# Kernel optimization log

Measured on AMD Instinct MI355X. Metric: run time of the kernel, lower is better.

The kernel has to match this reference:

```python
import jax, jax.numpy as jnp
import numpy as np
from jax import lax

QMAX = 127.0
EPS = 1e-8

T, B, I, H, L = 1024, 16, 1024, 1024, 2


def setup_inputs() -> dict:
    key = jax.random.key(0)
    ks = jax.random.split(key, 16)
    d = {
        "x": jax.random.normal(ks[0], (T, B, I), jnp.float32),
        "h0": jnp.zeros((L, B, H), jnp.float32),
        "c0": jnp.zeros((L, B, H), jnp.float32),
    }
    # layer 0 weights
    d["w_ih0"] = jax.random.normal(ks[1], (4 * H, I), jnp.float32) * 0.05
    d["w_hh0"] = jax.random.normal(ks[2], (4 * H, H), jnp.float32) * 0.05
    d["b_ih0"] = jax.random.normal(ks[3], (4 * H,), jnp.float32) * 0.05
    d["b_hh0"] = jax.random.normal(ks[4], (4 * H,), jnp.float32) * 0.05
    # layer 1 weights (layer_input_size == hidden_size)
    d["w_ih1"] = jax.random.normal(ks[5], (4 * H, H), jnp.float32) * 0.05
    d["w_hh1"] = jax.random.normal(ks[6], (4 * H, H), jnp.float32) * 0.05
    d["b_ih1"] = jax.random.normal(ks[7], (4 * H,), jnp.float32) * 0.05
    d["b_hh1"] = jax.random.normal(ks[8], (4 * H,), jnp.float32) * 0.05
    return d


def _quantize_weight(w):
    # per-tensor symmetric int8 quantization (simulates quantized.linear_prepack)
    s = jnp.maximum(jnp.max(jnp.abs(w)), EPS) / QMAX
    wq = jnp.clip(jnp.round(w / s), -QMAX, QMAX)  # integer values held in fp32
    return wq, s


def _dynq_matmul(x, wq, w_scale):
    # dynamic per-tensor activation quantization + int8xint8 matmul (fp32-emulated)
    x_scale = jnp.maximum(jnp.max(jnp.abs(x)), EPS) / QMAX
    xq = jnp.clip(jnp.round(x / x_scale), -QMAX, QMAX)
    return (xq @ wq.T) * (x_scale * w_scale)


def _lstm_layer(x, h0, c0, w_ih, w_hh, b_ih, b_hh):
    wq_ih, s_ih = _quantize_weight(w_ih)
    wq_hh, s_hh = _quantize_weight(w_hh)

    def step(carry, xt):
        h, c = carry
        gates = (_dynq_matmul(xt, wq_ih, s_ih) + b_ih
                 + _dynq_matmul(h, wq_hh, s_hh) + b_hh)  # [B, 4H]
        i, f, g, o = jnp.split(gates, 4, axis=-1)  # PyTorch gate order i,f,g,o
        i, f, o = jax.nn.sigmoid(i), jax.nn.sigmoid(f), jax.nn.sigmoid(o)
        g = jnp.tanh(g)
        c_new = f * c + i * g
        h_new = o * jnp.tanh(c_new)
        return (h_new, c_new), h_new

    (hT, cT), ys = lax.scan(step, (h0, c0), x)
    return ys, hT, cT


def reference(x, h0, c0, w_ih0, w_hh0, b_ih0, b_hh0, w_ih1, w_hh1, b_ih1, b_hh1):
    y, h_l0, c_l0 = _lstm_layer(x, h0[0], c0[0], w_ih0, w_hh0, b_ih0, b_hh0)
    y, h_l1, c_l1 = _lstm_layer(y, h0[1], c0[1], w_ih1, w_hh1, b_ih1, b_hh1)
    h_n = jnp.stack([h_l0, h_l1], axis=0)  # [L, B, H]
    c_n = jnp.stack([c_l0, c_l1], axis=0)
    return y, h_n, c_n
```

## Files before the change

kernel.cpp:

```cpp
#include <hip/hip_runtime.h>


#define T_STEPS 1024

typedef int v4i __attribute__((ext_vector_type(4)));
typedef float v4f __attribute__((ext_vector_type(4)));
typedef unsigned v2u __attribute__((ext_vector_type(2)));

#define DEV static __device__ __forceinline__

DEV float qclip(float v) { return fminf(fmaxf(v, -127.0f), 127.0f); }

DEV unsigned pack4i(float a, float b, float c, float d) {
  int ia = (int)a, ib = (int)b, ic = (int)c, id = (int)d;
  return (unsigned)(ia & 0xff) | ((unsigned)(ib & 0xff) << 8) |
         ((unsigned)(ic & 0xff) << 16) | ((unsigned)(id & 0xff) << 24);
}

DEV float qdiv(float v, float s) { return qclip(rintf(v / s)); }
DEV float qmul(float v, float inv) { return qclip(rintf(v * inv)); }

DEV v4i cloadi(const void* p) {
  v4i r;
  asm volatile("global_load_dwordx4 %0, %1, off sc0 sc1" : "=v"(r) : "v"(p) : "memory");
  return r;
}
DEV v4f cloadf(const void* p) {
  v4f r;
  asm volatile("global_load_dwordx4 %0, %1, off sc0 sc1" : "=v"(r) : "v"(p) : "memory");
  return r;
}
DEV unsigned cload4(const void* p) {
  unsigned r;
  asm volatile("global_load_dword %0, %1, off sc0 sc1" : "=v"(r) : "v"(p) : "memory");
  return r;
}
DEV v2u cload8w(const void* p) {
  v2u r;
  asm volatile("global_load_dwordx2 %0, %1, off sc0 sc1\n\ts_waitcnt vmcnt(0)"
               : "=v"(r) : "v"(p) : "memory");
  return r;
}
DEV void cstore16(void* p, v4f v) {
  asm volatile("global_store_dwordx4 %0, %1, off sc0 sc1" :: "v"(p), "v"(v) : "memory");
}
DEV void cstore8(void* p, v2u v) {
  asm volatile("global_store_dwordx2 %0, %1, off sc0 sc1" :: "v"(p), "v"(v) : "memory");
}
DEV void cstore4u(void* p, unsigned v) {
  asm volatile("global_store_dword %0, %1, off sc0 sc1" :: "v"(p), "v"(v) : "memory");
}
DEV void cstore4f(void* p, float v) {
  asm volatile("global_store_dword %0, %1, off sc0 sc1" :: "v"(p), "v"(v) : "memory");
}
DEV void vdone() {
  asm volatile("s_waitcnt vmcnt(0)" ::: "memory");
  __builtin_amdgcn_sched_barrier(0);
}

#define MFMA_I8 __builtin_amdgcn_mfma_i32_16x16x64_i8

__global__ void init_kernel(const float* __restrict__ h0in, char* __restrict__ ws) {
  const int layer = blockIdx.x;
  const int tid = threadIdx.x;
  const float* src = h0in + layer * 16384;
  char* ring = ws + (layer ? 196608 : 65536) + 65536;
  v2u* pubs = (v2u*)(ws + (layer ? 640 : 128)) + 32;
  for (int d = tid; d < 4096; d += 256) {
    int lb = d >> 7, b = (d >> 3) & 15, cq = (d & 7) << 2;
    v4f v = *(const v4f*)(src + (b << 10) + (lb << 5) + cq);
    cstore16(ring + ((size_t)d << 4), v);
  }
  __shared__ float red[256];
  const int lb = tid >> 3, su = tid & 7;
  float m = 0.0f;
  for (int b = su * 2; b < su * 2 + 2; ++b)
    for (int q = 0; q < 32; ++q) m = fmaxf(m, fabsf(src[b * 1024 + lb * 32 + q]));
  red[tid] = m;
  __syncthreads();
  if (su == 0) {
    float mm = red[tid];
#pragma unroll
    for (int i = 1; i < 8; ++i) mm = fmaxf(mm, red[tid + i]);
    v2u p;
    p.x = 0u;
    p.y = __float_as_uint(mm);
    cstore8((char*)&pubs[lb], p);
  }
}

__global__ void wabsmax_kernel(const float* __restrict__ w0, const float* __restrict__ w1,
                               const float* __restrict__ w2, const float* __restrict__ w3,
                               unsigned* wmax) {
  const int tensor = blockIdx.x >> 8;
  const int blk = blockIdx.x & 255;
  const float* w = tensor == 0 ? w0 : tensor == 1 ? w1 : tensor == 2 ? w2 : w3;
  const int tid = threadIdx.x;
  const float4* src = (const float4*)w;
  float m = 0.0f;
#pragma unroll
  for (int i = 0; i < 16; ++i) {
    float4 v = src[blk * 4096 + (i << 8) + tid];
    m = fmaxf(m, fmaxf(fmaxf(fabsf(v.x), fabsf(v.y)), fmaxf(fabsf(v.z), fabsf(v.w))));
  }
  __shared__ float red[256];
  red[tid] = m;
  __syncthreads();
  for (int off = 128; off > 0; off >>= 1) {
    if (tid < off) red[tid] = fmaxf(red[tid], red[tid + off]);
    __syncthreads();
  }
  if (tid == 0)
    __hip_atomic_fetch_max(&wmax[tensor], __float_as_uint(red[0]),
                           __ATOMIC_RELAXED, __HIP_MEMORY_SCOPE_AGENT);
}

__global__ void wquant_kernel(const float* __restrict__ w0, const float* __restrict__ w1,
                              const float* __restrict__ w2, const float* __restrict__ w3,
                              const unsigned* __restrict__ wmax,
                              unsigned char* __restrict__ wq) {
  const int tensor = blockIdx.x >> 12;
  const int blk = blockIdx.x & 4095;
  const float* w = tensor == 0 ? w0 : tensor == 1 ? w1 : tensor == 2 ? w2 : w3;
  const float s = fmaxf(__uint_as_float(wmax[tensor]), 1e-8f) / 127.0f;
  const int f4 = (blk << 8) + threadIdx.x;
  float4 v = ((const float4*)w)[f4];
  unsigned* dst = (unsigned*)(wq + (size_t)tensor * 4194304u);
  dst[f4] = pack4i(qdiv(v.x, s), qdiv(v.y, s), qdiv(v.z, s), qdiv(v.w, s));
}

__global__ void xquant_kernel(const float* __restrict__ x, float* __restrict__ xscale,
                              unsigned char* __restrict__ xq) {
  const int t = blockIdx.x;
  const int tid = threadIdx.x;
  const float4* src = (const float4*)(x + (size_t)t * 16384u);
  float4 vb[16];
  float m = 0.0f;
#pragma unroll
  for (int i = 0; i < 16; ++i) {
    float4 v = src[(i << 8) + tid];
    vb[i] = v;
    m = fmaxf(m, fmaxf(fmaxf(fabsf(v.x), fabsf(v.y)), fmaxf(fabsf(v.z), fabsf(v.w))));
  }
  __shared__ float red[256];
  red[tid] = m;
  __syncthreads();
  for (int off = 128; off > 0; off >>= 1) {
    if (tid < off) red[tid] = fmaxf(red[tid], red[tid + off]);
    __syncthreads();
  }
  __shared__ float ssh;
  if (tid == 0) {
    float s = fmaxf(red[0], 1e-8f) / 127.0f;
    xscale[t] = s;
    ssh = s;
  }
  __syncthreads();
  const float s = ssh;
  unsigned char* dst = xq + ((size_t)t << 14);
  const int kk = tid >> 4;
  const int hi = (tid >> 2) & 3;
  const int jo = (tid & 3) << 2;
#pragma unroll
  for (int i = 0; i < 16; ++i) {
    float4 v = vb[i];
    unsigned q = pack4i(qdiv(v.x, s), qdiv(v.y, s), qdiv(v.z, s), qdiv(v.w, s));
    *(unsigned*)(dst + (kk << 10) + ((i | (hi << 4)) << 4) + jo) = q;
  }
}

__global__ __launch_bounds__(512, 2) void seq_kernel(
    const unsigned char* __restrict__ xq, const float* __restrict__ xscale,
    const unsigned char* __restrict__ wq_base, const unsigned* __restrict__ wmax,
    const float* __restrict__ bih0, const float* __restrict__ bhh0,
    const float* __restrict__ bih1, const float* __restrict__ bhh1,
    char* __restrict__ ws, const float* __restrict__ c0in, float* __restrict__ dout) {
  const int blk = blockIdx.x;
  const int layer = blk >> 5;
  const int lb = blk & 31;
  const int j0 = lb << 5;
  const int tid = threadIdx.x;
  const int w = tid >> 6;
  const int lane = tid & 63;
  const int gate = (lane >> 2) & 3;
  const int unit_l = (w << 2) + (lane & 3);
  const int b0 = (lane >> 4) << 2;

  v2u* pubs0 = (v2u*)(ws + 128);
  v2u* pubs1 = (v2u*)(ws + 640);
  float* hmax0f = (float*)(ws + 4096);
  char* h0f = ws + 65536;
  char* h1f = ws + 196608;
  char* h0qp = ws + 327680;

  __shared__ __align__(16) unsigned char ahq[16][1040];
  __shared__ __align__(16) unsigned char axq[16][1040];
  __shared__ float hstash[16][33];
  __shared__ float redw[8];

  const unsigned char* wqi = wq_base + (size_t)(2 * layer) * 4194304u;
  const unsigned char* wqh = wq_base + (size_t)(2 * layer + 1) * 4194304u;
  const float s_wi = fmaxf(__uint_as_float(wmax[2 * layer + 0]), 1e-8f) / 127.0f;
  const float s_wh = fmaxf(__uint_as_float(wmax[2 * layer + 1]), 1e-8f) / 127.0f;

  const int ncol = (gate << 10) + j0 + unit_l;
  const int ksub = (lane >> 4) << 4;
  const int arow = lane & 15;
  const int gbase = lane & ~12;

  v4i wfi[16], wfh[16];
  {
    const unsigned char* pi = wqi + (size_t)ncol * 1024u + ksub;
    const unsigned char* ph = wqh + (size_t)ncol * 1024u + ksub;
#pragma unroll
    for (int kk = 0; kk < 16; ++kk) {
      wfi[kk] = *(const v4i*)(pi + (kk << 6));
      wfh[kk] = *(const v4i*)(ph + (kk << 6));
    }
  }
  const float bsum = (layer ? bih1 : bih0)[ncol] + (layer ? bhh1 : bhh0)[ncol];

  float cr[4];
#pragma unroll
  for (int r = 0; r < 4; ++r) cr[r] = c0in[(layer << 14) + ((b0 + r) << 10) + j0 + unit_l];

  float bm = 0.f;

  if (layer == 0) {
    for (int s = 0; s <= T_STEPS; ++s) {
      const bool full = (s < T_STEPS);
      v4i ax0 = {0, 0, 0, 0}, ax1 = {0, 0, 0, 0};
      float sxs = 0.f;
      if (full) {
        sxs = xscale[s];
        const unsigned char* xb = xq + ((size_t)s << 14) + (lane << 4);
        v4i xa[8];
#pragma unroll
        for (int kk = 0; kk < 8; ++kk) xa[kk] = *(const v4i*)(xb + (kk << 10));
#pragma unroll
        for (int kk = 0; kk < 8; kk += 2) {
          ax0 = MFMA_I8(xa[kk], wfi[kk], ax0, 0, 0, 0);
          ax1 = MFMA_I8(xa[kk + 1], wfi[kk + 1], ax1, 0, 0, 0);
        }
#pragma unroll
        for (int kk = 0; kk < 8; ++kk) xa[kk] = *(const v4i*)(xb + ((kk + 8) << 10));
#pragma unroll
        for (int kk = 0; kk < 8; kk += 2) {
          ax0 = MFMA_I8(xa[kk], wfi[kk + 8], ax0, 0, 0, 0);
          ax1 = MFMA_I8(xa[kk + 1], wfi[kk + 9], ax1, 0, 0, 0);
        }
      }
      const int slot = (s + 1) & 1;
      const v2u* pp = (lane < 32) ? (pubs0 + (slot << 5) + lane)
                                  : (pubs1 + (slot << 5) + (lane - 32));
      const unsigned tgt = (lane < 32) ? (unsigned)s
                                       : ((s >= 9) ? (unsigned)(s - 8) : 0u);
      v2u pv;
      unsigned guard = 0;
      for (;;) {
        pv = cload8w(pp);
        if (__ballot(pv.x >= tgt) == ~0ull) break;
        __builtin_amdgcn_s_sleep(1);
        if (++guard > (1u << 20)) break;
      }
      const char* hsrc = h0f + (size_t)slot * 65536;
      v4f hv[8];
#pragma unroll
      for (int i = 0; i < 8; ++i) hv[i] = cloadf(hsrc + (i << 13) + (tid << 4));
      float pm = __uint_as_float(pv.y);
#pragma unroll
      for (int m = 1; m < 32; m <<= 1) pm = fmaxf(pm, __shfl_xor(pm, m));
      const float gmax = __shfl(pm, 0);
      const float sh = fmaxf(gmax, 1e-8f) / 127.0f;
      const float inv = 1.0f / sh;
      vdone();
#pragma unroll
      for (int i = 0; i < 8; ++i) {
        unsigned uq = pack4i(qmul(hv[i].x, inv), qmul(hv[i].y, inv),
                             qmul(hv[i].z, inv), qmul(hv[i].w, inv));
        int o = (i << 13) + (tid << 4);
        int lbs = o >> 11, b = (o >> 7) & 15, c = (o & 127) >> 2;
        *(unsigned*)&ahq[b][(lbs << 5) + c] = uq;
      }
      __syncthreads();
      if (s > 0) {
        if (tid < 128) {
          int b = tid >> 3, c = (tid & 7) << 2;
          unsigned uq = *(const unsigned*)&ahq[b][j0 + c];
          cstore4u(h0qp + (size_t)((s - 1) & 7) * 16384 + (lb << 9) + (b << 5) + c, uq);
        }
        if (lb == 0 && tid == 256) cstore4f(&hmax0f[s - 1], gmax);
      }
      if (full) {
        v4i ah0 = {0, 0, 0, 0}, ah1 = {0, 0, 0, 0};
#pragma unroll
        for (int kk = 0; kk < 16; kk += 2) {
          v4i a = *(const v4i*)&ahq[arow][(kk << 6) + ksub];
          v4i b = *(const v4i*)&ahq[arow][((kk + 1) << 6) + ksub];
          ah0 = MFMA_I8(a, wfh[kk], ah0, 0, 0, 0);
          ah1 = MFMA_I8(b, wfh[kk + 1], ah1, 0, 0, 0);
        }
        const float fx = sxs * s_wi, fh = sh * s_wh;
        float am = 0.f;
#pragma unroll
        for (int r = 0; r < 4; ++r) {
          float gv = (float)(ax0[r] + ax1[r]) * fx + (float)(ah0[r] + ah1[r]) * fh + bsum;
          float xxv = (gate == 2) ? 2.f * gv : gv;
          float sg = __fdividef(1.f, 1.f + __expf(-xxv));
          float act = (gate == 2) ? 2.f * sg - 1.f : sg;
          float gi = __shfl(act, gbase);
          float gf = __shfl(act, gbase | 4);
          float gg = __shfl(act, gbase | 8);
          float go = __shfl(act, gbase | 12);
          float cn = gf * cr[r] + gi * gg;
          cr[r] = cn;
          float h = go * (2.f * __fdividef(1.f, 1.f + __expf(-2.f * cn)) - 1.f);
          if (gate == 0) hstash[b0 + r][unit_l] = h;
          am = fmaxf(am, fabsf(h));
        }
#pragma unroll
        for (int m = 1; m < 64; m <<= 1) am = fmaxf(am, __shfl_xor(am, m));
        if (lane == 0) redw[w] = am;
        __syncthreads();
        if (tid < 128) {
          int b = tid >> 3, c = (tid & 7) << 2;
          v4f hw = {hstash[b][c], hstash[b][c + 1], hstash[b][c + 2], hstash[b][c + 3]};
          cstore16(h0f + (size_t)(s & 1) * 65536 + (lb << 11) + (b << 7) + (c << 2), hw);
          if (s == T_STEPS - 1)
            *(v4f*)(dout + 16777216u + (b << 10) + j0 + c) = hw;
        }
        if (tid == 0) {
          bm = redw[0];
#pragma unroll
          for (int i = 1; i < 8; ++i) bm = fmaxf(bm, redw[i]);
        }
      }
      vdone();
      __syncthreads();
      if (tid == 0) {
        v2u pub;
        pub.x = (unsigned)(s + 1);
        pub.y = __float_as_uint(bm);
        cstore8((char*)(pubs0 + ((s & 1) << 5) + lb), pub);
      }
    }
    if (gate == 0) {
#pragma unroll
      for (int r = 0; r < 4; ++r)
        dout[16777216u + 32768u + ((b0 + r) << 10) + j0 + unit_l] = cr[r];
    }
  } else {
    for (int u = 0; u < T_STEPS; ++u) {
      const int slot = (u + 1) & 1;
      const v2u* pp = (lane < 32) ? (pubs0 + (slot << 5) + lane)
                                  : (pubs1 + (slot << 5) + (lane - 32));
      const unsigned tgt = (lane < 32) ? (unsigned)(u + 2) : (unsigned)u;
      v2u pv;
      unsigned guard = 0;
      for (;;) {
        pv = cload8w(pp);
        if (__ballot(pv.x >= tgt) == ~0ull) break;
        __builtin_amdgcn_s_sleep(1);
        if (++guard > (1u << 20)) break;
      }
      const char* qsrc = h0qp + (size_t)(u & 7) * 16384;
      v4i q0 = cloadi(qsrc + (tid << 4));
      v4i q1 = cloadi(qsrc + 8192 + (tid << 4));
      const char* hsrc = h1f + (size_t)slot * 65536;
      v4f hv[8];
#pragma unroll
      for (int i = 0; i < 8; ++i) hv[i] = cloadf(hsrc + (i << 13) + (tid << 4));
      unsigned sxb = cload4(&hmax0f[u]);
      float pm = __uint_as_float(pv.y);
#pragma unroll
      for (int m = 1; m < 32; m <<= 1) pm = fmaxf(pm, __shfl_xor(pm, m));
      const float gmax1 = __shfl(pm, 32);
      const float sh = fmaxf(gmax1, 1e-8f) / 127.0f;
      const float inv = 1.0f / sh;
      vdone();
      const float sxs = fmaxf(__uint_as_float(sxb), 1e-8f) / 127.0f;
      {
        int o = tid << 4;
        *(v4i*)&axq[(o >> 5) & 15][((o >> 9) << 5) + (o & 31)] = q0;
        int o1 = o + 8192;
        *(v4i*)&axq[(o1 >> 5) & 15][((o1 >> 9) << 5) + (o1 & 31)] = q1;
      }
#pragma unroll
      for (int i = 0; i < 8; ++i) {
        unsigned uq = pack4i(qmul(hv[i].x, inv), qmul(hv[i].y, inv),
                             qmul(hv[i].z, inv), qmul(hv[i].w, inv));
        int o = (i << 13) + (tid << 4);
        int lbs = o >> 11, b = (o >> 7) & 15, c = (o & 127) >> 2;
        *(unsigned*)&ahq[b][(lbs << 5) + c] = uq;
      }
      __syncthreads();
      v4i ax0 = {0, 0, 0, 0}, ax1 = {0, 0, 0, 0};
      v4i ah0 = {0, 0, 0, 0}, ah1 = {0, 0, 0, 0};
#pragma unroll
      for (int kk = 0; kk < 16; kk += 2) {
        v4i a0 = *(const v4i*)&axq[arow][(kk << 6) + ksub];
        v4i a1 = *(const v4i*)&axq[arow][((kk + 1) << 6) + ksub];
        v4i b0v = *(const v4i*)&ahq[arow][(kk << 6) + ksub];
        v4i b1v = *(const v4i*)&ahq[arow][((kk + 1) << 6) + ksub];
        ax0 = MFMA_I8(a0, wfi[kk], ax0, 0, 0, 0);
        ax1 = MFMA_I8(a1, wfi[kk + 1], ax1, 0, 0, 0);
        ah0 = MFMA_I8(b0v, wfh[kk], ah0, 0, 0, 0);
        ah1 = MFMA_I8(b1v, wfh[kk + 1], ah1, 0, 0, 0);
      }
      const float fx = sxs * s_wi, fh = sh * s_wh;
      float am = 0.f;
#pragma unroll
      for (int r = 0; r < 4; ++r) {
        float gv = (float)(ax0[r] + ax1[r]) * fx + (float)(ah0[r] + ah1[r]) * fh + bsum;
        float xxv = (gate == 2) ? 2.f * gv : gv;
        float sg = __fdividef(1.f, 1.f + __expf(-xxv));
        float act = (gate == 2) ? 2.f * sg - 1.f : sg;
        float gi = __shfl(act, gbase);
        float gf = __shfl(act, gbase | 4);
        float gg = __shfl(act, gbase | 8);
        float go = __shfl(act, gbase | 12);
        float cn = gf * cr[r] + gi * gg;
        cr[r] = cn;
        float h = go * (2.f * __fdividef(1.f, 1.f + __expf(-2.f * cn)) - 1.f);
        if (gate == 0) hstash[b0 + r][unit_l] = h;
        am = fmaxf(am, fabsf(h));
      }
#pragma unroll
      for (int m = 1; m < 64; m <<= 1) am = fmaxf(am, __shfl_xor(am, m));
      if (lane == 0) redw[w] = am;
      __syncthreads();
      if (tid < 128) {
        int b = tid >> 3, c = (tid & 7) << 2;
        v4f hw = {hstash[b][c], hstash[b][c + 1], hstash[b][c + 2], hstash[b][c + 3]};
        cstore16(h1f + (size_t)(u & 1) * 65536 + (lb << 11) + (b << 7) + (c << 2), hw);
        *(v4f*)(dout + ((size_t)u << 14) + (b << 10) + j0 + c) = hw;
        if (u == T_STEPS - 1)
          *(v4f*)(dout + 16777216u + 16384u + (b << 10) + j0 + c) = hw;
      }
      if (tid == 0) {
        bm = redw[0];
#pragma unroll
        for (int i = 1; i < 8; ++i) bm = fmaxf(bm, redw[i]);
      }
      vdone();
      __syncthreads();
      if (tid == 0) {
        v2u pub;
        pub.x = (unsigned)(u + 1);
        pub.y = __float_as_uint(bm);
        cstore8((char*)(pubs1 + ((u & 1) << 5) + lb), pub);
      }
    }
    if (gate == 0) {
#pragma unroll
      for (int r = 0; r < 4; ++r)
        dout[16777216u + 32768u + 16384u + ((b0 + r) << 10) + j0 + unit_l] = cr[r];
    }
  }
}

extern "C" void kernel_launch(void* const* d_in, const int* in_sizes, int n_in,
                              void* d_out, int out_size, void* d_ws, size_t ws_size,
                              hipStream_t stream) {
  (void)in_sizes; (void)n_in; (void)out_size; (void)ws_size;
  const float* x     = (const float*)d_in[0];
  const float* h0in  = (const float*)d_in[1];
  const float* c0in  = (const float*)d_in[2];
  const float* w_ih0 = (const float*)d_in[3];
  const float* w_hh0 = (const float*)d_in[4];
  const float* b_ih0 = (const float*)d_in[5];
  const float* b_hh0 = (const float*)d_in[6];
  const float* w_ih1 = (const float*)d_in[7];
  const float* w_hh1 = (const float*)d_in[8];
  const float* b_ih1 = (const float*)d_in[9];
  const float* b_hh1 = (const float*)d_in[10];

  char* ws = (char*)d_ws;
  unsigned* wmax   = (unsigned*)(ws + 0);
  float* xscale    = (float*)(ws + 8192);
  unsigned char* wqb = (unsigned char*)(ws + (1u << 20));
  unsigned char* xq  = (unsigned char*)(ws + (1u << 20) + 4u * 4194304u);

  hipMemsetAsync(ws, 0, 65536, stream);
  hipLaunchKernelGGL(init_kernel, dim3(2), dim3(256), 0, stream, h0in, ws);
  hipLaunchKernelGGL(wabsmax_kernel, dim3(1024), dim3(256), 0, stream,
                     w_ih0, w_hh0, w_ih1, w_hh1, wmax);
  hipLaunchKernelGGL(wquant_kernel, dim3(16384), dim3(256), 0, stream,
                     w_ih0, w_hh0, w_ih1, w_hh1, wmax, wqb);
  hipLaunchKernelGGL(xquant_kernel, dim3(1024), dim3(256), 0, stream,
                     x, xscale, xq);
  hipLaunchKernelGGL(seq_kernel, dim3(64), dim3(512), 0, stream,
                     xq, xscale, wqb, wmax,
                     b_ih0, b_hh0, b_ih1, b_hh1,
                     ws, c0in, (float*)d_out);
}
```

Before: 5.759 ms.

## Exchange pre-quantized int8 hidden state with per-word tags instead of fp32 plus barriers

Before, each block published its fp32 hidden-state slice, then did a store-drain and block barrier before a publish flag. Consumers loaded the full fp32 state and quantized it themselves. Now each block publishes only its absmax first. Once consumers have the global max, each block quantizes its own slice and writes int8 words paired with a step tag into a deeper 8-slot ring. Consumers poll the ring until every tag matches, which removes the vmcnt drain and the extra barrier before publishing and cuts the bytes exchanged per step. The cost is an extra polling loop over the ring, a deeper pipeline of publish slots (4-slot pubs), and reliance on 8-byte stores being atomic.

```diff
diff --git a/kernel.cpp b/kernel.cpp
--- a/kernel.cpp
+++ b/kernel.cpp
@@ -20,19 +20,9 @@
 DEV float qdiv(float v, float s) { return qclip(rintf(v / s)); }
 DEV float qmul(float v, float inv) { return qclip(rintf(v * inv)); }
 
-DEV v4i cloadi(const void* p) {
-  v4i r;
-  asm volatile("global_load_dwordx4 %0, %1, off sc0 sc1" : "=v"(r) : "v"(p) : "memory");
-  return r;
-}
-DEV v4f cloadf(const void* p) {
-  v4f r;
-  asm volatile("global_load_dwordx4 %0, %1, off sc0 sc1" : "=v"(r) : "v"(p) : "memory");
-  return r;
-}
-DEV unsigned cload4(const void* p) {
-  unsigned r;
-  asm volatile("global_load_dword %0, %1, off sc0 sc1" : "=v"(r) : "v"(p) : "memory");
+DEV v2u cloadi2(const void* p) {
+  v2u r;
+  asm volatile("global_load_dwordx2 %0, %1, off sc0 sc1" : "=v"(r) : "v"(p) : "memory");
   return r;
 }
 DEV v2u cload8w(const void* p) {
@@ -41,17 +31,8 @@
                : "=v"(r) : "v"(p) : "memory");
   return r;
 }
-DEV void cstore16(void* p, v4f v) {
-  asm volatile("global_store_dwordx4 %0, %1, off sc0 sc1" :: "v"(p), "v"(v) : "memory");
-}
 DEV void cstore8(void* p, v2u v) {
   asm volatile("global_store_dwordx2 %0, %1, off sc0 sc1" :: "v"(p), "v"(v) : "memory");
-}
-DEV void cstore4u(void* p, unsigned v) {
-  asm volatile("global_store_dword %0, %1, off sc0 sc1" :: "v"(p), "v"(v) : "memory");
-}
-DEV void cstore4f(void* p, float v) {
-  asm volatile("global_store_dword %0, %1, off sc0 sc1" :: "v"(p), "v"(v) : "memory");
 }
 DEV void vdone() {
   asm volatile("s_waitcnt vmcnt(0)" ::: "memory");
@@ -64,16 +45,12 @@
   const int layer = blockIdx.x;
   const int tid = threadIdx.x;
   const float* src = h0in + layer * 16384;
-  char* ring = ws + (layer ? 196608 : 65536) + 65536;
-  v2u* pubs = (v2u*)(ws + (layer ? 640 : 128)) + 32;
-  for (int d = tid; d < 4096; d += 256) {
-    int lb = d >> 7, b = (d >> 3) & 15, cq = (d & 7) << 2;
-    v4f v = *(const v4f*)(src + (b << 10) + (lb << 5) + cq);
-    cstore16(ring + ((size_t)d << 4), v);
-  }
+  char* ring = ws + 65536 + layer * 262144 + 32768;
+  v2u* pubs = (v2u*)(ws + 128 + layer * 1024) + 32;
   __shared__ float red[256];
+  __shared__ float chmax[32];
   const int lb = tid >> 3, su = tid & 7;
-  float m = 0.0f;
+  float m = 0.f;
   for (int b = su * 2; b < su * 2 + 2; ++b)
     for (int q = 0; q < 32; ++q) m = fmaxf(m, fabsf(src[b * 1024 + lb * 32 + q]));
   red[tid] = m;
@@ -82,10 +59,24 @@
     float mm = red[tid];
 #pragma unroll
     for (int i = 1; i < 8; ++i) mm = fmaxf(mm, red[tid + i]);
+    chmax[lb] = mm;
     v2u p;
-    p.x = 0u;
+    p.x = 1u;
     p.y = __float_as_uint(mm);
     cstore8((char*)&pubs[lb], p);
+  }
+  __syncthreads();
+  float gm = chmax[0];
+  for (int i = 1; i < 32; ++i) gm = fmaxf(gm, chmax[i]);
+  const float s = fmaxf(gm, 1e-8f) / 127.0f;
+  for (int i = 0; i < 16; ++i) {
+    int G = tid + (i << 8);
+    int glb = G >> 7, g = G & 127, b = g >> 3, cg = g & 7;
+    const float* v = src + b * 1024 + glb * 32 + (cg << 2);
+    v2u gr;
+    gr.x = pack4i(qdiv(v[0], s), qdiv(v[1], s), qdiv(v[2], s), qdiv(v[3], s));
+    gr.y = 1u;
+    cstore8(ring + (G << 3), gr);
   }
 }
 
@@ -187,11 +178,9 @@
   const int b0 = (lane >> 4) << 2;
 
   v2u* pubs0 = (v2u*)(ws + 128);
-  v2u* pubs1 = (v2u*)(ws + 640);
-  float* hmax0f = (float*)(ws + 4096);
-  char* h0f = ws + 65536;
-  char* h1f = ws + 196608;
-  char* h0qp = ws + 327680;
+  v2u* pubs1 = (v2u*)(ws + 1152);
+  char* ring0 = ws + 65536;
+  char* ring1 = ws + 65536 + 262144;
 
   __shared__ __align__(16) unsigned char ahq[16][1040];
   __shared__ __align__(16) unsigned char axq[16][1040];
@@ -223,8 +212,6 @@
   float cr[4];
 #pragma unroll
   for (int r = 0; r < 4; ++r) cr[r] = c0in[(layer << 14) + ((b0 + r) << 10) + j0 + unit_l];
-
-  float bm = 0.f;
 
   if (layer == 0) {
     for (int s = 0; s <= T_STEPS; ++s) {
@@ -250,48 +237,66 @@
           ax1 = MFMA_I8(xa[kk + 1], wfi[kk + 9], ax1, 0, 0, 0);
         }
       }
-      const int slot = (s + 1) & 1;
-      const v2u* pp = (lane < 32) ? (pubs0 + (slot << 5) + lane)
-                                  : (pubs1 + (slot << 5) + (lane - 32));
-      const unsigned tgt = (lane < 32) ? (unsigned)s
-                                       : ((s >= 9) ? (unsigned)(s - 8) : 0u);
+      const unsigned ptag = (unsigned)(s + 1);
+      int gs = s - 2;
+      if (gs < 0) gs = 0;
+      const v2u* pp = (lane < 32) ? (pubs0 + (((s + 1) & 3) << 5) + lane)
+                                  : (pubs1 + ((gs & 3) << 5) + (lane - 32));
+      const unsigned etag = (lane < 32) ? ptag : (unsigned)gs;
       v2u pv;
       unsigned guard = 0;
       for (;;) {
         pv = cload8w(pp);
-        if (__ballot(pv.x >= tgt) == ~0ull) break;
+        if (__ballot(pv.x == etag) == ~0ull) break;
         __builtin_amdgcn_s_sleep(1);
         if (++guard > (1u << 20)) break;
       }
-      const char* hsrc = h0f + (size_t)slot * 65536;
-      v4f hv[8];
-#pragma unroll
-      for (int i = 0; i < 8; ++i) hv[i] = cloadf(hsrc + (i << 13) + (tid << 4));
-      float pm = __uint_as_float(pv.y);
-#pragma unroll
-      for (int m = 1; m < 32; m <<= 1) pm = fmaxf(pm, __shfl_xor(pm, m));
-      const float gmax = __shfl(pm, 0);
-      const float sh = fmaxf(gmax, 1e-8f) / 127.0f;
+      float pm = (lane < 32) ? __uint_as_float(pv.y) : -1e30f;
+#pragma unroll
+      for (int m = 1; m < 64; m <<= 1) pm = fmaxf(pm, __shfl_xor(pm, m));
+      const float sh = fmaxf(pm, 1e-8f) / 127.0f;
       const float inv = 1.0f / sh;
-      vdone();
-#pragma unroll
-      for (int i = 0; i < 8; ++i) {
-        unsigned uq = pack4i(qmul(hv[i].x, inv), qmul(hv[i].y, inv),
-                             qmul(hv[i].z, inv), qmul(hv[i].w, inv));
-        int o = (i << 13) + (tid << 4);
-        int lbs = o >> 11, b = (o >> 7) & 15, c = (o & 127) >> 2;
-        *(unsigned*)&ahq[b][(lbs << 5) + c] = uq;
-      }
-      __syncthreads();
-      if (s > 0) {
-        if (tid < 128) {
-          int b = tid >> 3, c = (tid & 7) << 2;
-          unsigned uq = *(const unsigned*)&ahq[b][j0 + c];
-          cstore4u(h0qp + (size_t)((s - 1) & 7) * 16384 + (lb << 9) + (b << 5) + c, uq);
-        }
-        if (lb == 0 && tid == 256) cstore4f(&hmax0f[s - 1], gmax);
+
+      const int dslot = (s + 1) & 7;
+      char* rb = ring0 + dslot * 32768;
+      if (s > 0 && tid < 128) {
+        int b = tid >> 3, cg = tid & 7;
+        unsigned q = pack4i(qmul(hstash[b][(cg << 2)], inv),
+                            qmul(hstash[b][(cg << 2) + 1], inv),
+                            qmul(hstash[b][(cg << 2) + 2], inv),
+                            qmul(hstash[b][(cg << 2) + 3], inv));
+        *(unsigned*)&ahq[b][j0 + (cg << 2)] = q;
+        v2u gr;
+        gr.x = q;
+        gr.y = ptag;
+        cstore8(rb + (((lb << 7) + tid) << 3), gr);
       }
       if (full) {
+        v2u gv[8];
+        unsigned guard2 = 0;
+        for (;;) {
+#pragma unroll
+          for (int i = 0; i < 8; ++i) gv[i] = cloadi2(rb + ((tid + (i << 9)) << 3));
+          vdone();
+          unsigned good = 1u;
+#pragma unroll
+          for (int i = 0; i < 8; ++i) {
+            int G = tid + (i << 9);
+            bool own = ((G >> 7) == lb) && (s > 0);
+            good &= (own || gv[i].y == ptag) ? 1u : 0u;
+          }
+          if (__ballot(good != 0u) == ~0ull) break;
+          __builtin_amdgcn_s_sleep(1);
+          if (++guard2 > (1u << 20)) break;
+        }
+#pragma unroll
+        for (int i = 0; i < 8; ++i) {
+          int G = tid + (i << 9);
+          int glb = G >> 7, g = G & 127;
+          if (!((glb == lb) && (s > 0)))
+            *(unsigned*)&ahq[g >> 3][(glb << 5) + ((g & 7) << 2)] = gv[i].x;
+        }
+        __syncthreads();
         v4i ah0 = {0, 0, 0, 0}, ah1 = {0, 0, 0, 0};
 #pragma unroll
         for (int kk = 0; kk < 16; kk += 2) {
@@ -304,8 +309,8 @@
         float am = 0.f;
 #pragma unroll
         for (int r = 0; r < 4; ++r) {
-          float gv = (float)(ax0[r] + ax1[r]) * fx + (float)(ah0[r] + ah1[r]) * fh + bsum;
-          float xxv = (gate == 2) ? 2.f * gv : gv;
+          float gv2 = (float)(ax0[r] + ax1[r]) * fx + (float)(ah0[r] + ah1[r]) * fh + bsum;
+          float xxv = (gate == 2) ? 2.f * gv2 : gv2;
           float sg = __fdividef(1.f, 1.f + __expf(-xxv));
           float act = (gate == 2) ? 2.f * sg - 1.f : sg;
           float gi = __shfl(act, gbase);
@@ -322,26 +327,20 @@
         for (int m = 1; m < 64; m <<= 1) am = fmaxf(am, __shfl_xor(am, m));
         if (lane == 0) redw[w] = am;
         __syncthreads();
-        if (tid < 128) {
+        if (tid < 128 && s == T_STEPS - 1) {
           int b = tid >> 3, c = (tid & 7) << 2;
           v4f hw = {hstash[b][c], hstash[b][c + 1], hstash[b][c + 2], hstash[b][c + 3]};
-          cstore16(h0f + (size_t)(s & 1) * 65536 + (lb << 11) + (b << 7) + (c << 2), hw);
-          if (s == T_STEPS - 1)
-            *(v4f*)(dout + 16777216u + (b << 10) + j0 + c) = hw;
+          *(v4f*)(dout + 16777216u + (b << 10) + j0 + c) = hw;
         }
         if (tid == 0) {
-          bm = redw[0];
+          float bm = redw[0];
 #pragma unroll
           for (int i = 1; i < 8; ++i) bm = fmaxf(bm, redw[i]);
-        }
-      }
-      vdone();
-      __syncthreads();
-      if (tid == 0) {
-        v2u pub;
-        pub.x = (unsigned)(s + 1);
-        pub.y = __float_as_uint(bm);
-        cstore8((char*)(pubs0 + ((s & 1) << 5) + lb), pub);
+          v2u pub;
+          pub.x = (unsigned)(s + 2);
+          pub.y = __float_as_uint(bm);
+          cstore8((char*)(pubs0 + (((s + 2) & 3) << 5) + lb), pub);
+        }
       }
     }
     if (gate == 0) {
@@ -351,47 +350,67 @@
     }
   } else {
     for (int u = 0; u < T_STEPS; ++u) {
-      const int slot = (u + 1) & 1;
-      const v2u* pp = (lane < 32) ? (pubs0 + (slot << 5) + lane)
-                                  : (pubs1 + (slot << 5) + (lane - 32));
-      const unsigned tgt = (lane < 32) ? (unsigned)(u + 2) : (unsigned)u;
+      const unsigned xtag = (unsigned)(u + 2);
+      const unsigned htag = (unsigned)(u + 1);
+      const v2u* pp = (lane < 32) ? (pubs0 + (((u + 2) & 3) << 5) + lane)
+                                  : (pubs1 + (((u + 1) & 3) << 5) + (lane - 32));
+      const unsigned etag = (lane < 32) ? xtag : htag;
       v2u pv;
       unsigned guard = 0;
       for (;;) {
         pv = cload8w(pp);
-        if (__ballot(pv.x >= tgt) == ~0ull) break;
+        if (__ballot(pv.x == etag) == ~0ull) break;
         __builtin_amdgcn_s_sleep(1);
         if (++guard > (1u << 20)) break;
       }
-      const char* qsrc = h0qp + (size_t)(u & 7) * 16384;
-      v4i q0 = cloadi(qsrc + (tid << 4));
-      v4i q1 = cloadi(qsrc + 8192 + (tid << 4));
-      const char* hsrc = h1f + (size_t)slot * 65536;
-      v4f hv[8];
-#pragma unroll
-      for (int i = 0; i < 8; ++i) hv[i] = cloadf(hsrc + (i << 13) + (tid << 4));
-      unsigned sxb = cload4(&hmax0f[u]);
       float pm = __uint_as_float(pv.y);
 #pragma unroll
       for (int m = 1; m < 32; m <<= 1) pm = fmaxf(pm, __shfl_xor(pm, m));
-      const float gmax1 = __shfl(pm, 32);
-      const float sh = fmaxf(gmax1, 1e-8f) / 127.0f;
+      const float sxs = fmaxf(__shfl(pm, 0), 1e-8f) / 127.0f;
+      const float sh = fmaxf(__shfl(pm, 32), 1e-8f) / 127.0f;
       const float inv = 1.0f / sh;
-      vdone();
-      const float sxs = fmaxf(__uint_as_float(sxb), 1e-8f) / 127.0f;
-      {
-        int o = tid << 4;
-        *(v4i*)&axq[(o >> 5) & 15][((o >> 9) << 5) + (o & 31)] = q0;
-        int o1 = o + 8192;
-        *(v4i*)&axq[(o1 >> 5) & 15][((o1 >> 9) << 5) + (o1 & 31)] = q1;
+
+      char* rb1 = ring1 + (((u + 1) & 7)) * 32768;
+      const char* rb0 = ring0 + (((u + 2) & 7)) * 32768;
+      if (u > 0 && tid < 128) {
+        int b = tid >> 3, cg = tid & 7;
+        unsigned q = pack4i(qmul(hstash[b][(cg << 2)], inv),
+                            qmul(hstash[b][(cg << 2) + 1], inv),
+                            qmul(hstash[b][(cg << 2) + 2], inv),
+                            qmul(hstash[b][(cg << 2) + 3], inv));
+        *(unsigned*)&ahq[b][j0 + (cg << 2)] = q;
+        v2u gr;
+        gr.x = q;
+        gr.y = htag;
+        cstore8(rb1 + (((lb << 7) + tid) << 3), gr);
+      }
+      v2u gv[16];
+      unsigned guard2 = 0;
+      for (;;) {
+#pragma unroll
+        for (int i = 0; i < 8; ++i) gv[i] = cloadi2(rb1 + ((tid + (i << 9)) << 3));
+#pragma unroll
+        for (int i = 0; i < 8; ++i) gv[8 + i] = cloadi2(rb0 + ((tid + (i << 9)) << 3));
+        vdone();
+        unsigned good = 1u;
+#pragma unroll
+        for (int i = 0; i < 8; ++i) {
+          int G = tid + (i << 9);
+          bool own = ((G >> 7) == lb) && (u > 0);
+          good &= (own || gv[i].y == htag) ? 1u : 0u;
+          good &= (gv[8 + i].y == xtag) ? 1u : 0u;
+        }
+        if (__ballot(good != 0u) == ~0ull) break;
+        __builtin_amdgcn_s_sleep(1);
+        if (++guard2 > (1u << 20)) break;
       }
 #pragma unroll
       for (int i = 0; i < 8; ++i) {
-        unsigned uq = pack4i(qmul(hv[i].x, inv), qmul(hv[i].y, inv),
-                             qmul(hv[i].z, inv), qmul(hv[i].w, inv));
-        int o = (i << 13) + (tid << 4);
-        int lbs = o >> 11, b = (o >> 7) & 15, c = (o & 127) >> 2;
-        *(unsigned*)&ahq[b][(lbs << 5) + c] = uq;
+        int G = tid + (i << 9);
+        int glb = G >> 7, g = G & 127;
+        if (!((glb == lb) && (u > 0)))
+          *(unsigned*)&ahq[g >> 3][(glb << 5) + ((g & 7) << 2)] = gv[i].x;
+        *(unsigned*)&axq[g >> 3][(glb << 5) + ((g & 7) << 2)] = gv[8 + i].x;
       }
       __syncthreads();
       v4i ax0 = {0, 0, 0, 0}, ax1 = {0, 0, 0, 0};
@@ -411,8 +430,8 @@
       float am = 0.f;
 #pragma unroll
       for (int r = 0; r < 4; ++r) {
-        float gv = (float)(ax0[r] + ax1[r]) * fx + (float)(ah0[r] + ah1[r]) * fh + bsum;
-        float xxv = (gate == 2) ? 2.f * gv : gv;
+        float gv2 = (float)(ax0[r] + ax1[r]) * fx + (float)(ah0[r] + ah1[r]) * fh + bsum;
+        float xxv = (gate == 2) ? 2.f * gv2 : gv2;
         float sg = __fdividef(1.f, 1.f + __expf(-xxv));
         float act = (gate == 2) ? 2.f * sg - 1.f : sg;
         float gi = __shfl(act, gbase);
@@ -432,23 +451,18 @@
       if (tid < 128) {
         int b = tid >> 3, c = (tid & 7) << 2;
         v4f hw = {hstash[b][c], hstash[b][c + 1], hstash[b][c + 2], hstash[b][c + 3]};
-        cstore16(h1f + (size_t)(u & 1) * 65536 + (lb << 11) + (b << 7) + (c << 2), hw);
         *(v4f*)(dout + ((size_t)u << 14) + (b << 10) + j0 + c) = hw;
         if (u == T_STEPS - 1)
           *(v4f*)(dout + 16777216u + 16384u + (b << 10) + j0 + c) = hw;
       }
       if (tid == 0) {
-        bm = redw[0];
+        float bm = redw[0];
 #pragma unroll
         for (int i = 1; i < 8; ++i) bm = fmaxf(bm, redw[i]);
-      }
-      vdone();
-      __syncthreads();
-      if (tid == 0) {
         v2u pub;
-        pub.x = (unsigned)(u + 1);
+        pub.x = (unsigned)(u + 2);
         pub.y = __float_as_uint(bm);
-        cstore8((char*)(pubs1 + ((u & 1) << 5) + lb), pub);
+        cstore8((char*)(pubs1 + (((u + 2) & 3) << 5) + lb), pub);
       }
     }
     if (gate == 0) {
```

New measurement: 6.504 ms. +12.9%, slower.
